# Performance work log

Hardware: AMD Instinct MI355X
Metric: run time of the kernel (lower is better)

Reference implementation:

```python
import jax, jax.numpy as jnp
import numpy as np

B, T, C = 4, 2048, 1024
N_HEAD = 16
HEAD_DIM = C // N_HEAD
SCALE = 1.0 / np.sqrt(HEAD_DIM).astype(np.float32)


def setup_inputs() -> dict:
    key = jax.random.key(0)
    k1, k2, k3 = jax.random.split(key, 3)
    x = jax.random.normal(k1, (B, T, C), dtype=jnp.float32)
    # torch Linear weights: [out_features, in_features], scaled init
    w_qkv = jax.random.normal(k2, (3 * C, C), dtype=jnp.float32) * (1.0 / np.sqrt(C))
    w_out = jax.random.normal(k3, (C, C), dtype=jnp.float32) * (1.0 / np.sqrt(C))
    b_out = jnp.zeros((C,), dtype=jnp.float32)
    return {"x": x, "w_qkv": w_qkv, "w_out": w_out, "b_out": b_out}


def reference(x, w_qkv, w_out, b_out):
    Bsz, Tlen, Cdim = x.shape
    qkv = jnp.einsum('btc,oc->bto', x, w_qkv)  # [B,T,3C]
    q, k, v = jnp.split(qkv, 3, axis=-1)
    # [B,H,T,D]
    def heads(t):
        return t.reshape(Bsz, Tlen, N_HEAD, HEAD_DIM).transpose(0, 2, 1, 3)
    q, k, v = heads(q), heads(k), heads(v)
    att = jnp.einsum('bhqd,bhkd->bhqk', q, k) * SCALE  # [B,H,T,T]
    causal = jnp.tril(jnp.ones((Tlen, Tlen), dtype=bool))
    att = jnp.where(causal[None, None], att, -jnp.inf)
    att = jax.nn.softmax(att, axis=-1)
    out = jnp.einsum('bhqk,bhkd->bhqd', att, v)
    out = out.transpose(0, 2, 1, 3).reshape(Bsz, Tlen, Cdim)
    out = jnp.einsum('btc,oc->bto', out, w_out) + b_out
    return out
```

## Files before the change

### kernel.cpp

```cpp
#include <hip/hip_runtime.h>
#include <stdint.h>


typedef __attribute__((ext_vector_type(8))) short bf16x8;
typedef __attribute__((ext_vector_type(4))) float f32x4;

#define EXP2F(x) __builtin_amdgcn_exp2f(x)
#define SL2E 0.18033688011112042f
#define FIXED_M 15.0f

template <bool B> struct BoolC { static constexpr bool value = B; };
template <int I> struct IntC { static constexpr int value = I; };

__device__ __forceinline__ short f2bf(float f) {
  union { float f; unsigned u; } c; c.f = f;
  unsigned u = c.u;
  unsigned r = (u + 0x7fffu + ((u >> 16) & 1u)) >> 16;
  return (short)(unsigned short)r;
}

__device__ __forceinline__ void softmax_pack(const f32x4* sc, bf16x8& pa0, bf16x8& pa1) {
  union U { int i[4]; bf16x8 v; };
  U u0, u1;
#pragma unroll
  for (int j = 0; j < 4; ++j) {
    float p0 = EXP2F(sc[j][0]);
    float p1 = EXP2F(sc[j][1]);
    float p2 = EXP2F(sc[j][2]);
    float p3 = EXP2F(sc[j][3]);
    int w0, w1;
    asm("v_cvt_pk_bf16_f32 %0, %1, %2" : "=v"(w0) : "v"(p0), "v"(p1));
    asm("v_cvt_pk_bf16_f32 %0, %1, %2" : "=v"(w1) : "v"(p2), "v"(p3));
    if (j < 2) { u0.i[j * 2] = w0; u0.i[j * 2 + 1] = w1; }
    else       { u1.i[(j - 2) * 2] = w0; u1.i[(j - 2) * 2 + 1] = w1; }
  }
  pa0 = u0.v;
  pa1 = u1.v;
}

__device__ __forceinline__ void llds16(const short* g, short* l) {
  __builtin_amdgcn_global_load_lds(
      (const __attribute__((address_space(1))) unsigned int*)g,
      (__attribute__((address_space(3))) unsigned int*)l, 16, 0, 0);
}

__global__ __launch_bounds__(256) void cast_all(
    const float* __restrict__ x, const float* __restrict__ wq,
    const float* __restrict__ wo, short* __restrict__ xb,
    short* __restrict__ wqb, short* __restrict__ wob) {
  const int b = blockIdx.x;
  const float* src;
  short* dst;
  int idx;
  if (b < 8192)        { src = x;  dst = xb;  idx = b * 256 + threadIdx.x; }
  else if (b < 11264)  { src = wq; dst = wqb; idx = (b - 8192) * 256 + threadIdx.x; }
  else                 { src = wo; dst = wob; idx = (b - 11264) * 256 + threadIdx.x; }
  float4 f = ((const float4*)src)[idx];
  short4 o;
  o.x = f2bf(f.x); o.y = f2bf(f.y); o.z = f2bf(f.z); o.w = f2bf(f.w);
  ((short4*)dst)[idx] = o;
}

__global__ __launch_bounds__(512) void gemm_qkv(
    const short* __restrict__ A, const short* __restrict__ Bw,
    short* __restrict__ Qo, short* __restrict__ Ko, short* __restrict__ Vt) {
  const int K = 1024;
  __shared__ short smem[73728];
  const int tid = threadIdx.x;
  const int lane = tid & 63;
  const int wave = tid >> 6;
  const int wr = wave >> 1;
  const int wc = wave & 1;
  const int m0 = blockIdx.y * 256;
  const int n0 = blockIdx.x * 128;
  const int mrow = lane & 15;
  const int kq = lane >> 4;

  f32x4 acc[4][4];
#pragma unroll
  for (int i = 0; i < 4; ++i)
#pragma unroll
    for (int j = 0; j < 4; ++j) acc[i][j] = (f32x4){0.f, 0.f, 0.f, 0.f};

  auto stageA = [&](int t, int buf, int ca) {
    const int c = ca * 512 + tid;
    const int row = c >> 3;
    const int sc = (c & 7) ^ (row & 7);
    llds16(A + (size_t)(m0 + row) * K + t * 64 + sc * 8,
           &smem[buf * 24576 + c * 8]);
  };
  auto stageB = [&](int t, int buf, int cb) {
    const int c = cb * 512 + tid;
    const int row = c >> 3;
    const int sc = (c & 7) ^ (row & 7);
    llds16(Bw + (size_t)(n0 + row) * K + t * 64 + sc * 8,
           &smem[buf * 24576 + 16384 + c * 8]);
  };

  auto rdA = [&](const short* lA, int i, int kk) -> bf16x8 {
    const int row = wr * 64 + i * 16 + mrow;
    const int ch = (kq + 4 * kk) ^ (row & 7);
    return *(const bf16x8*)&lA[row * 64 + ch * 8];
  };
  auto rdB = [&](const short* lB, int j, int kk) -> bf16x8 {
    const int row = wc * 64 + j * 16 + mrow;
    const int ch = (kq + 4 * kk) ^ (row & 7);
    return *(const bf16x8*)&lB[row * 64 + ch * 8];
  };

  stageA(0, 0, 0); stageA(0, 0, 1); stageA(0, 0, 2); stageA(0, 0, 3);
  stageB(0, 0, 0); stageB(0, 0, 1);
  stageA(1, 1, 0); stageA(1, 1, 1); stageA(1, 1, 2); stageA(1, 1, 3);
  stageB(1, 1, 0); stageB(1, 1, 1);
  asm volatile("s_waitcnt vmcnt(6)" ::: "memory");
  __builtin_amdgcn_s_barrier();

#define PHASE_TAIL()                                         \
  __builtin_amdgcn_s_barrier();                              \
  asm volatile("s_waitcnt lgkmcnt(0)" ::: "memory");         \
  __builtin_amdgcn_sched_barrier(0);                         \
  __builtin_amdgcn_s_setprio(1);

#define PHASE_END()                                          \
  __builtin_amdgcn_s_setprio(0);                             \
  __builtin_amdgcn_sched_barrier(0);                         \
  __builtin_amdgcn_s_barrier();

  for (int t = 0; t < 16; ++t) {
    const int bufi = t % 3;
    const int nb = (t + 2) % 3;
    const short* lA = &smem[bufi * 24576];
    const short* lB = lA + 16384;
    bf16x8 a0, a1, a2, a3, bf0, bf1, bf2, bf3;

    a0 = rdA(lA, 0, 0); a1 = rdA(lA, 1, 0);
    bf0 = rdB(lB, 0, 0); bf1 = rdB(lB, 1, 0);
    bf2 = rdB(lB, 2, 0); bf3 = rdB(lB, 3, 0);
    if (t < 14) { stageA(t + 2, nb, 0); stageA(t + 2, nb, 1); }
    PHASE_TAIL();
    acc[0][0] = __builtin_amdgcn_mfma_f32_16x16x32_bf16(a0, bf0, acc[0][0], 0, 0, 0);
    acc[0][1] = __builtin_amdgcn_mfma_f32_16x16x32_bf16(a0, bf1, acc[0][1], 0, 0, 0);
    acc[0][2] = __builtin_amdgcn_mfma_f32_16x16x32_bf16(a0, bf2, acc[0][2], 0, 0, 0);
    acc[0][3] = __builtin_amdgcn_mfma_f32_16x16x32_bf16(a0, bf3, acc[0][3], 0, 0, 0);
    acc[1][0] = __builtin_amdgcn_mfma_f32_16x16x32_bf16(a1, bf0, acc[1][0], 0, 0, 0);
    acc[1][1] = __builtin_amdgcn_mfma_f32_16x16x32_bf16(a1, bf1, acc[1][1], 0, 0, 0);
    acc[1][2] = __builtin_amdgcn_mfma_f32_16x16x32_bf16(a1, bf2, acc[1][2], 0, 0, 0);
    acc[1][3] = __builtin_amdgcn_mfma_f32_16x16x32_bf16(a1, bf3, acc[1][3], 0, 0, 0);
    PHASE_END();

    a2 = rdA(lA, 2, 0); a3 = rdA(lA, 3, 0);
    if (t < 14) { stageA(t + 2, nb, 2); stageA(t + 2, nb, 3); }
    PHASE_TAIL();
    acc[2][0] = __builtin_amdgcn_mfma_f32_16x16x32_bf16(a2, bf0, acc[2][0], 0, 0, 0);
    acc[2][1] = __builtin_amdgcn_mfma_f32_16x16x32_bf16(a2, bf1, acc[2][1], 0, 0, 0);
    acc[2][2] = __builtin_amdgcn_mfma_f32_16x16x32_bf16(a2, bf2, acc[2][2], 0, 0, 0);
    acc[2][3] = __builtin_amdgcn_mfma_f32_16x16x32_bf16(a2, bf3, acc[2][3], 0, 0, 0);
    acc[3][0] = __builtin_amdgcn_mfma_f32_16x16x32_bf16(a3, bf0, acc[3][0], 0, 0, 0);
    acc[3][1] = __builtin_amdgcn_mfma_f32_16x16x32_bf16(a3, bf1, acc[3][1], 0, 0, 0);
    acc[3][2] = __builtin_amdgcn_mfma_f32_16x16x32_bf16(a3, bf2, acc[3][2], 0, 0, 0);
    acc[3][3] = __builtin_amdgcn_mfma_f32_16x16x32_bf16(a3, bf3, acc[3][3], 0, 0, 0);
    PHASE_END();

    a0 = rdA(lA, 0, 1); a1 = rdA(lA, 1, 1);
    bf0 = rdB(lB, 0, 1); bf1 = rdB(lB, 1, 1);
    bf2 = rdB(lB, 2, 1); bf3 = rdB(lB, 3, 1);
    if (t < 14) { stageB(t + 2, nb, 0); stageB(t + 2, nb, 1); }
    PHASE_TAIL();
    acc[0][0] = __builtin_amdgcn_mfma_f32_16x16x32_bf16(a0, bf0, acc[0][0], 0, 0, 0);
    acc[0][1] = __builtin_amdgcn_mfma_f32_16x16x32_bf16(a0, bf1, acc[0][1], 0, 0, 0);
    acc[0][2] = __builtin_amdgcn_mfma_f32_16x16x32_bf16(a0, bf2, acc[0][2], 0, 0, 0);
    acc[0][3] = __builtin_amdgcn_mfma_f32_16x16x32_bf16(a0, bf3, acc[0][3], 0, 0, 0);
    acc[1][0] = __builtin_amdgcn_mfma_f32_16x16x32_bf16(a1, bf0, acc[1][0], 0, 0, 0);
    acc[1][1] = __builtin_amdgcn_mfma_f32_16x16x32_bf16(a1, bf1, acc[1][1], 0, 0, 0);
    acc[1][2] = __builtin_amdgcn_mfma_f32_16x16x32_bf16(a1, bf2, acc[1][2], 0, 0, 0);
    acc[1][3] = __builtin_amdgcn_mfma_f32_16x16x32_bf16(a1, bf3, acc[1][3], 0, 0, 0);
    PHASE_END();

    a2 = rdA(lA, 2, 1); a3 = rdA(lA, 3, 1);
    PHASE_TAIL();
    acc[2][0] = __builtin_amdgcn_mfma_f32_16x16x32_bf16(a2, bf0, acc[2][0], 0, 0, 0);
    acc[2][1] = __builtin_amdgcn_mfma_f32_16x16x32_bf16(a2, bf1, acc[2][1], 0, 0, 0);
    acc[2][2] = __builtin_amdgcn_mfma_f32_16x16x32_bf16(a2, bf2, acc[2][2], 0, 0, 0);
    acc[2][3] = __builtin_amdgcn_mfma_f32_16x16x32_bf16(a2, bf3, acc[2][3], 0, 0, 0);
    acc[3][0] = __builtin_amdgcn_mfma_f32_16x16x32_bf16(a3, bf0, acc[3][0], 0, 0, 0);
    acc[3][1] = __builtin_amdgcn_mfma_f32_16x16x32_bf16(a3, bf1, acc[3][1], 0, 0, 0);
    acc[3][2] = __builtin_amdgcn_mfma_f32_16x16x32_bf16(a3, bf2, acc[3][2], 0, 0, 0);
    acc[3][3] = __builtin_amdgcn_mfma_f32_16x16x32_bf16(a3, bf3, acc[3][3], 0, 0, 0);
    __builtin_amdgcn_s_setprio(0);
    __builtin_amdgcn_sched_barrier(0);
    if (t <= 13)      asm volatile("s_waitcnt vmcnt(6)" ::: "memory");
    else if (t == 14) asm volatile("s_waitcnt vmcnt(0)" ::: "memory");
    __builtin_amdgcn_s_barrier();
  }
#undef PHASE_TAIL
#undef PHASE_END

  __syncthreads();

  const int b = m0 >> 11;
  if (n0 < 2048) {
    const float sc_ = ((n0 >> 10) == 1) ? SL2E : 1.0f;
    short* lC = smem;
#pragma unroll
    for (int i = 0; i < 4; ++i) {
      const int rl = wr * 64 + i * 16 + kq * 4;
#pragma unroll
      for (int j = 0; j < 4; ++j) {
        const int col = wc * 64 + j * 16 + mrow;
#pragma unroll
        for (int r = 0; r < 4; ++r)
          lC[(rl + r) * 132 + col] = f2bf(acc[i][j][r] * sc_);
      }
    }
    __syncthreads();
    short* dst = (n0 >> 10) == 0 ? Qo : Ko;
#pragma unroll
    for (int call = 0; call < 8; ++call) {
      const int cc = call * 512 + tid;
      const int row = cc >> 4;
      const int ch = cc & 15;
      const int t = (m0 & 2047) + row;
      const int c = (n0 + ch * 8) & 1023;
      const int h = c >> 6;
      const int d = c & 63;
      bf16x8 val = *(const bf16x8*)&lC[row * 132 + ch * 8];
      *(bf16x8*)(dst + ((size_t)(b * 16 + h) * 2048 + t) * 64 + d) = val;
    }
  } else {
    short* lCt = smem;
#pragma unroll
    for (int i = 0; i < 4; ++i) {
      const int rl = wr * 64 + i * 16 + kq * 4;
#pragma unroll
      for (int j = 0; j < 4; ++j) {
        const int col = wc * 64 + j * 16 + mrow;
#pragma unroll
        for (int r = 0; r < 4; ++r)
          lCt[col * 264 + rl + r] = f2bf(acc[i][j][r]);
      }
    }
    __syncthreads();
#pragma unroll
    for (int call = 0; call < 8; ++call) {
      const int cc = call * 512 + tid;
      const int col = cc >> 5;
      const int tg = cc & 31;
      const int o = n0 + col;
      const int d = o & 63;
      const int h = (o >> 6) & 15;
      const int t = (m0 & 2047) + tg * 8;
      bf16x8 val = *(const bf16x8*)&lCt[col * 264 + tg * 8];
      *(bf16x8*)(Vt + ((size_t)(b * 16 + h) * 64 + d) * 2048 + t) = val;
    }
  }
}

__global__ __launch_bounds__(512) void gemm_out(
    const short* __restrict__ A, const short* __restrict__ Bw,
    const float* __restrict__ bias, float* __restrict__ Out) {
  const int K = 1024;
  __shared__ short smem[73728];
  const int tid = threadIdx.x;
  const int lane = tid & 63;
  const int wave = tid >> 6;
  const int wr = wave >> 1;
  const int wc = wave & 1;
  const int m0 = blockIdx.y * 256;
  const int n0 = blockIdx.x * 128;
  const int mrow = lane & 15;
  const int kq = lane >> 4;

  f32x4 acc[4][4];
#pragma unroll
  for (int i = 0; i < 4; ++i)
#pragma unroll
    for (int j = 0; j < 4; ++j) acc[i][j] = (f32x4){0.f, 0.f, 0.f, 0.f};

  auto stageA = [&](int t, int buf, int ca) {
    const int c = ca * 512 + tid;
    const int row = c >> 3;
    const int sc = (c & 7) ^ (row & 7);
    llds16(A + (size_t)(m0 + row) * K + t * 64 + sc * 8,
           &smem[buf * 24576 + c * 8]);
  };
  auto stageB = [&](int t, int buf, int cb) {
    const int c = cb * 512 + tid;
    const int row = c >> 3;
    const int sc = (c & 7) ^ (row & 7);
    llds16(Bw + (size_t)(n0 + row) * K + t * 64 + sc * 8,
           &smem[buf * 24576 + 16384 + c * 8]);
  };

  auto rdA = [&](const short* lA, int i, int kk) -> bf16x8 {
    const int row = wr * 64 + i * 16 + mrow;
    const int ch = (kq + 4 * kk) ^ (row & 7);
    return *(const bf16x8*)&lA[row * 64 + ch * 8];
  };
  auto rdB = [&](const short* lB, int j, int kk) -> bf16x8 {
    const int row = wc * 64 + j * 16 + mrow;
    const int ch = (kq + 4 * kk) ^ (row & 7);
    return *(const bf16x8*)&lB[row * 64 + ch * 8];
  };

  stageA(0, 0, 0); stageA(0, 0, 1); stageA(0, 0, 2); stageA(0, 0, 3);
  stageB(0, 0, 0); stageB(0, 0, 1);
  stageA(1, 1, 0); stageA(1, 1, 1); stageA(1, 1, 2); stageA(1, 1, 3);
  stageB(1, 1, 0); stageB(1, 1, 1);
  asm volatile("s_waitcnt vmcnt(6)" ::: "memory");
  __builtin_amdgcn_s_barrier();

#define PHASE_TAIL()                                         \
  __builtin_amdgcn_s_barrier();                              \
  asm volatile("s_waitcnt lgkmcnt(0)" ::: "memory");         \
  __builtin_amdgcn_sched_barrier(0);                         \
  __builtin_amdgcn_s_setprio(1);

#define PHASE_END()                                          \
  __builtin_amdgcn_s_setprio(0);                             \
  __builtin_amdgcn_sched_barrier(0);                         \
  __builtin_amdgcn_s_barrier();

  for (int t = 0; t < 16; ++t) {
    const int bufi = t % 3;
    const int nb = (t + 2) % 3;
    const short* lA = &smem[bufi * 24576];
    const short* lB = lA + 16384;
    bf16x8 a0, a1, a2, a3, bf0, bf1, bf2, bf3;

    a0 = rdA(lA, 0, 0); a1 = rdA(lA, 1, 0);
    bf0 = rdB(lB, 0, 0); bf1 = rdB(lB, 1, 0);
    bf2 = rdB(lB, 2, 0); bf3 = rdB(lB, 3, 0);
    if (t < 14) { stageA(t + 2, nb, 0); stageA(t + 2, nb, 1); }
    PHASE_TAIL();
    acc[0][0] = __builtin_amdgcn_mfma_f32_16x16x32_bf16(a0, bf0, acc[0][0], 0, 0, 0);
    acc[0][1] = __builtin_amdgcn_mfma_f32_16x16x32_bf16(a0, bf1, acc[0][1], 0, 0, 0);
    acc[0][2] = __builtin_amdgcn_mfma_f32_16x16x32_bf16(a0, bf2, acc[0][2], 0, 0, 0);
    acc[0][3] = __builtin_amdgcn_mfma_f32_16x16x32_bf16(a0, bf3, acc[0][3], 0, 0, 0);
    acc[1][0] = __builtin_amdgcn_mfma_f32_16x16x32_bf16(a1, bf0, acc[1][0], 0, 0, 0);
    acc[1][1] = __builtin_amdgcn_mfma_f32_16x16x32_bf16(a1, bf1, acc[1][1], 0, 0, 0);
    acc[1][2] = __builtin_amdgcn_mfma_f32_16x16x32_bf16(a1, bf2, acc[1][2], 0, 0, 0);
    acc[1][3] = __builtin_amdgcn_mfma_f32_16x16x32_bf16(a1, bf3, acc[1][3], 0, 0, 0);
    PHASE_END();

    a2 = rdA(lA, 2, 0); a3 = rdA(lA, 3, 0);
    if (t < 14) { stageA(t + 2, nb, 2); stageA(t + 2, nb, 3); }
    PHASE_TAIL();
    acc[2][0] = __builtin_amdgcn_mfma_f32_16x16x32_bf16(a2, bf0, acc[2][0], 0, 0, 0);
    acc[2][1] = __builtin_amdgcn_mfma_f32_16x16x32_bf16(a2, bf1, acc[2][1], 0, 0, 0);
    acc[2][2] = __builtin_amdgcn_mfma_f32_16x16x32_bf16(a2, bf2, acc[2][2], 0, 0, 0);
    acc[2][3] = __builtin_amdgcn_mfma_f32_16x16x32_bf16(a2, bf3, acc[2][3], 0, 0, 0);
    acc[3][0] = __builtin_amdgcn_mfma_f32_16x16x32_bf16(a3, bf0, acc[3][0], 0, 0, 0);
    acc[3][1] = __builtin_amdgcn_mfma_f32_16x16x32_bf16(a3, bf1, acc[3][1], 0, 0, 0);
    acc[3][2] = __builtin_amdgcn_mfma_f32_16x16x32_bf16(a3, bf2, acc[3][2], 0, 0, 0);
    acc[3][3] = __builtin_amdgcn_mfma_f32_16x16x32_bf16(a3, bf3, acc[3][3], 0, 0, 0);
    PHASE_END();

    a0 = rdA(lA, 0, 1); a1 = rdA(lA, 1, 1);
    bf0 = rdB(lB, 0, 1); bf1 = rdB(lB, 1, 1);
    bf2 = rdB(lB, 2, 1); bf3 = rdB(lB, 3, 1);
    if (t < 14) { stageB(t + 2, nb, 0); stageB(t + 2, nb, 1); }
    PHASE_TAIL();
    acc[0][0] = __builtin_amdgcn_mfma_f32_16x16x32_bf16(a0, bf0, acc[0][0], 0, 0, 0);
    acc[0][1] = __builtin_amdgcn_mfma_f32_16x16x32_bf16(a0, bf1, acc[0][1], 0, 0, 0);
    acc[0][2] = __builtin_amdgcn_mfma_f32_16x16x32_bf16(a0, bf2, acc[0][2], 0, 0, 0);
    acc[0][3] = __builtin_amdgcn_mfma_f32_16x16x32_bf16(a0, bf3, acc[0][3], 0, 0, 0);
    acc[1][0] = __builtin_amdgcn_mfma_f32_16x16x32_bf16(a1, bf0, acc[1][0], 0, 0, 0);
    acc[1][1] = __builtin_amdgcn_mfma_f32_16x16x32_bf16(a1, bf1, acc[1][1], 0, 0, 0);
    acc[1][2] = __builtin_amdgcn_mfma_f32_16x16x32_bf16(a1, bf2, acc[1][2], 0, 0, 0);
    acc[1][3] = __builtin_amdgcn_mfma_f32_16x16x32_bf16(a1, bf3, acc[1][3], 0, 0, 0);
    PHASE_END();

    a2 = rdA(lA, 2, 1); a3 = rdA(lA, 3, 1);
    PHASE_TAIL();
    acc[2][0] = __builtin_amdgcn_mfma_f32_16x16x32_bf16(a2, bf0, acc[2][0], 0, 0, 0);
    acc[2][1] = __builtin_amdgcn_mfma_f32_16x16x32_bf16(a2, bf1, acc[2][1], 0, 0, 0);
    acc[2][2] = __builtin_amdgcn_mfma_f32_16x16x32_bf16(a2, bf2, acc[2][2], 0, 0, 0);
    acc[2][3] = __builtin_amdgcn_mfma_f32_16x16x32_bf16(a2, bf3, acc[2][3], 0, 0, 0);
    acc[3][0] = __builtin_amdgcn_mfma_f32_16x16x32_bf16(a3, bf0, acc[3][0], 0, 0, 0);
    acc[3][1] = __builtin_amdgcn_mfma_f32_16x16x32_bf16(a3, bf1, acc[3][1], 0, 0, 0);
    acc[3][2] = __builtin_amdgcn_mfma_f32_16x16x32_bf16(a3, bf2, acc[3][2], 0, 0, 0);
    acc[3][3] = __builtin_amdgcn_mfma_f32_16x16x32_bf16(a3, bf3, acc[3][3], 0, 0, 0);
    __builtin_amdgcn_s_setprio(0);
    __builtin_amdgcn_sched_barrier(0);
    if (t <= 13)      asm volatile("s_waitcnt vmcnt(6)" ::: "memory");
    else if (t == 14) asm volatile("s_waitcnt vmcnt(0)" ::: "memory");
    __builtin_amdgcn_s_barrier();
  }
#undef PHASE_TAIL
#undef PHASE_END

#pragma unroll
  for (int i = 0; i < 4; ++i) {
    const int m = m0 + wr * 64 + i * 16 + kq * 4;
#pragma unroll
    for (int j = 0; j < 4; ++j) {
      const int n = n0 + wc * 64 + j * 16 + mrow;
      const float bb = bias[n];
#pragma unroll
      for (int r = 0; r < 4; ++r)
        Out[(size_t)(m + r) * 1024 + n] = acc[i][j][r] + bb;
    }
  }
}

__global__ __launch_bounds__(256) void flash_attn(
    const short* __restrict__ Qg, const short* __restrict__ Kg,
    const short* __restrict__ Vtg, short* __restrict__ Og) {
  const int T = 2048;
  __shared__ short lK[2][64 * 64];
  __shared__ short lVt[2][64 * 64];
  const int tid = threadIdx.x;
  const int lane = tid & 63;
  const int wave = tid >> 6;
  const int bh = blockIdx.x;
  const int bx = blockIdx.y;
  const int mrow = lane & 15;
  const int kq = lane >> 4;
  const int swz = mrow & 7;
  const size_t base = (size_t)bh * T * 64;
  const size_t vbase = (size_t)bh * 64 * T;

  int qts[4];
  qts[0] = bx;
  qts[1] = 31 - bx;
  qts[2] = 15 - bx;
  qts[3] = 16 + bx;

  const bf16x8 ones = {0x3F80, 0x3F80, 0x3F80, 0x3F80, 0x3F80, 0x3F80, 0x3F80, 0x3F80};

  bf16x8 aq0[4], aq1[4];
#pragma unroll
  for (int s = 0; s < 4; ++s) {
    const short* qp = Qg + base + (size_t)(qts[s] * 64 + wave * 16 + mrow) * 64 + kq * 8;
    aq0[s] = *(const bf16x8*)qp;
    aq1[s] = *(const bf16x8*)(qp + 32);
  }

  f32x4 acc[4][4], lac[4];
#pragma unroll
  for (int s = 0; s < 4; ++s) {
    lac[s] = (f32x4){0.f, 0.f, 0.f, 0.f};
#pragma unroll
    for (int jd = 0; jd < 4; ++jd) acc[s][jd] = (f32x4){0.f, 0.f, 0.f, 0.f};
  }

  auto stage = [&](int nt, int buf) {
#pragma unroll
    for (int call = 0; call < 2; ++call) {
      const int cb = call * 256 + wave * 64;
      const int c = cb + lane;
      const int row = c >> 3;
      const int scol = (c & 7) ^ (row & 7);
      const int grow = (row & 0x23) | ((row & 0x0C) << 1) | ((row & 0x10) >> 2);
      llds16(Kg + base + (size_t)(nt * 64 + grow) * 64 + scol * 8, &lK[buf][cb * 8]);
      llds16(Vtg + vbase + (size_t)row * T + nt * 64 + scol * 8, &lVt[buf][cb * 8]);
    }
  };

  auto seg = [&](auto Aa, auto Pi, const short* K_, const short* Vt_, int kt) {
    constexpr bool ACT0 = decltype(Aa)::value;
    constexpr int pi = decltype(Pi)::value;
    f32x4 sc0[4], sc1[4];
#pragma unroll
    for (int j = 0; j < 4; ++j) {
      const short* krow = &K_[(j * 16 + mrow) * 64];
      bf16x8 kb0 = *(const bf16x8*)&krow[(kq ^ swz) * 8];
      bf16x8 kb1 = *(const bf16x8*)&krow[((4 + kq) ^ swz) * 8];
      __builtin_amdgcn_s_setprio(1);
      f32x4 ss = (f32x4){-FIXED_M, -FIXED_M, -FIXED_M, -FIXED_M};
      ss = __builtin_amdgcn_mfma_f32_16x16x32_bf16(kb0, aq0[pi + 1], ss, 0, 0, 0);
      ss = __builtin_amdgcn_mfma_f32_16x16x32_bf16(kb1, aq1[pi + 1], ss, 0, 0, 0);
      sc1[j] = ss;
      if constexpr (ACT0) {
        f32x4 s2 = (f32x4){-FIXED_M, -FIXED_M, -FIXED_M, -FIXED_M};
        s2 = __builtin_amdgcn_mfma_f32_16x16x32_bf16(kb0, aq0[pi], s2, 0, 0, 0);
        s2 = __builtin_amdgcn_mfma_f32_16x16x32_bf16(kb1, aq1[pi], s2, 0, 0, 0);
        sc0[j] = s2;
      }
      __builtin_amdgcn_s_setprio(0);
    }

    if (kt == qts[pi + 1]) {
      const int qcol = qts[pi + 1] * 64 + wave * 16 + mrow;
#pragma unroll
      for (int j = 0; j < 4; ++j) {
        const int keyb = kt * 64 + ((j & 2) << 4) + (kq << 3) + ((j & 1) << 2);
#pragma unroll
        for (int r = 0; r < 4; ++r)
          if (keyb + r > qcol) sc1[j][r] = -1e30f;
      }
    }
    if constexpr (ACT0) {
      if (kt == qts[pi]) {
        const int qcol = qts[pi] * 64 + wave * 16 + mrow;
#pragma unroll
        for (int j = 0; j < 4; ++j) {
          const int keyb = kt * 64 + ((j & 2) << 4) + (kq << 3) + ((j & 1) << 2);
#pragma unroll
          for (int r = 0; r < 4; ++r)
            if (keyb + r > qcol) sc0[j][r] = -1e30f;
        }
      }
    }

    bf16x8 pa0_1, pa1_1, pa0_0, pa1_0;
    softmax_pack(sc1, pa0_1, pa1_1);
    lac[pi + 1] = __builtin_amdgcn_mfma_f32_16x16x32_bf16(pa0_1, ones, lac[pi + 1], 0, 0, 0);
    lac[pi + 1] = __builtin_amdgcn_mfma_f32_16x16x32_bf16(pa1_1, ones, lac[pi + 1], 0, 0, 0);
    if constexpr (ACT0) {
      softmax_pack(sc0, pa0_0, pa1_0);
      lac[pi] = __builtin_amdgcn_mfma_f32_16x16x32_bf16(pa0_0, ones, lac[pi], 0, 0, 0);
      lac[pi] = __builtin_amdgcn_mfma_f32_16x16x32_bf16(pa1_0, ones, lac[pi], 0, 0, 0);
    }

#pragma unroll
    for (int jd = 0; jd < 4; ++jd) {
      const short* vrow = &Vt_[(jd * 16 + mrow) * 64];
      bf16x8 vb0 = *(const bf16x8*)&vrow[(kq ^ swz) * 8];
      bf16x8 vb1 = *(const bf16x8*)&vrow[((4 + kq) ^ swz) * 8];
      __builtin_amdgcn_s_setprio(1);
      acc[pi + 1][jd] = __builtin_amdgcn_mfma_f32_16x16x32_bf16(pa0_1, vb0, acc[pi + 1][jd], 0, 0, 0);
      acc[pi + 1][jd] = __builtin_amdgcn_mfma_f32_16x16x32_bf16(pa1_1, vb1, acc[pi + 1][jd], 0, 0, 0);
      if constexpr (ACT0) {
        acc[pi][jd] = __builtin_amdgcn_mfma_f32_16x16x32_bf16(pa0_0, vb0, acc[pi][jd], 0, 0, 0);
        acc[pi][jd] = __builtin_amdgcn_mfma_f32_16x16x32_bf16(pa1_0, vb1, acc[pi][jd], 0, 0, 0);
      }
      __builtin_amdgcn_s_setprio(0);
    }
  };

  stage(0, 0);
  const int ktmax = qts[1];
  for (int kt = 0; kt <= ktmax; ++kt) {
    const int bcur = kt & 1;
    if (kt < ktmax) {
      stage(kt + 1, bcur ^ 1);
      asm volatile("s_waitcnt vmcnt(4)" ::: "memory");
    } else {
      asm volatile("s_waitcnt vmcnt(0)" ::: "memory");
    }
    __builtin_amdgcn_s_barrier();
    const short* K_ = lK[bcur];
    const short* Vt_ = lVt[bcur];
    if (kt <= qts[0]) seg(BoolC<true>{}, IntC<0>{}, K_, Vt_, kt);
    else              seg(BoolC<false>{}, IntC<0>{}, K_, Vt_, kt);
    if (kt <= qts[3]) {
      if (kt <= qts[2]) seg(BoolC<true>{}, IntC<1 * 2>{}, K_, Vt_, kt);
      else              seg(BoolC<false>{}, IntC<1 * 2>{}, K_, Vt_, kt);
    }
    __builtin_amdgcn_s_barrier();
  }

  const int b = bh >> 4;
  const int h = bh & 15;
#pragma unroll
  for (int s = 0; s < 4; ++s) {
#pragma unroll
    for (int r = 0; r < 4; ++r) {
      const float inv = 1.0f / lac[s][r];
      const int t = qts[s] * 64 + wave * 16 + kq * 4 + r;
#pragma unroll
      for (int jd = 0; jd < 4; ++jd) {
        const int col = h * 64 + jd * 16 + mrow;
        Og[((size_t)b * 2048 + t) * 1024 + col] = f2bf(acc[s][jd][r] * inv);
      }
    }
  }
}

extern "C" void kernel_launch(void* const* d_in, const int* in_sizes, int n_in,
                              void* d_out, int out_size, void* d_ws, size_t ws_size,
                              hipStream_t stream) {
  const float* x = (const float*)d_in[0];
  const float* w_qkv = (const float*)d_in[1];
  const float* w_out = (const float*)d_in[2];
  const float* b_out = (const float*)d_in[3];
  float* out = (float*)d_out;

  char* ws = (char*)d_ws;
  const size_t NX = 8192ull * 1024;
  const size_t NWQ = 3072ull * 1024;
  const size_t NWO = 1024ull * 1024;
  const size_t NQ = 64ull * 2048 * 64;
  size_t off = 0;
  short* xb    = (short*)(ws + off); off += NX * 2;
  short* wqkvb = (short*)(ws + off); off += NWQ * 2;
  short* woutb = (short*)(ws + off); off += NWO * 2;
  short* q     = (short*)(ws + off); off += NQ * 2;
  short* k     = (short*)(ws + off); off += NQ * 2;
  short* vt    = (short*)(ws + off); off += NQ * 2;
  short* attb  = (short*)(ws + off); off += NX * 2;
  if (off > ws_size) return;

  cast_all<<<12288, 256, 0, stream>>>(x, w_qkv, w_out, xb, wqkvb, woutb);
  gemm_qkv<<<dim3(24, 32), 512, 0, stream>>>(xb, wqkvb, q, k, vt);
  flash_attn<<<dim3(64, 8), 256, 0, stream>>>(q, k, vt, attb);
  gemm_out<<<dim3(8, 32), 512, 0, stream>>>(attb, woutb, b_out, out);
}
```

Baseline: 243.0 us.

## Enlarge QKV GEMM tile to 256x256 with double-buffered LDS pipeline

```diff
diff --git a/kernel.cpp b/kernel.cpp
--- a/kernel.cpp
+++ b/kernel.cpp
@@ -65,20 +65,20 @@
     const short* __restrict__ A, const short* __restrict__ Bw,
     short* __restrict__ Qo, short* __restrict__ Ko, short* __restrict__ Vt) {
   const int K = 1024;
-  __shared__ short smem[73728];
+  __shared__ short smem[65536];
   const int tid = threadIdx.x;
   const int lane = tid & 63;
   const int wave = tid >> 6;
-  const int wr = wave >> 1;
-  const int wc = wave & 1;
+  const int wr = wave >> 2;
+  const int wc = wave & 3;
   const int m0 = blockIdx.y * 256;
-  const int n0 = blockIdx.x * 128;
+  const int n0 = blockIdx.x * 256;
   const int mrow = lane & 15;
   const int kq = lane >> 4;
 
-  f32x4 acc[4][4];
-#pragma unroll
-  for (int i = 0; i < 4; ++i)
+  f32x4 acc[8][4];
+#pragma unroll
+  for (int i = 0; i < 8; ++i)
 #pragma unroll
     for (int j = 0; j < 4; ++j) acc[i][j] = (f32x4){0.f, 0.f, 0.f, 0.f};
 
@@ -87,18 +87,18 @@
     const int row = c >> 3;
     const int sc = (c & 7) ^ (row & 7);
     llds16(A + (size_t)(m0 + row) * K + t * 64 + sc * 8,
-           &smem[buf * 24576 + c * 8]);
+           &smem[buf * 32768 + c * 8]);
   };
   auto stageB = [&](int t, int buf, int cb) {
     const int c = cb * 512 + tid;
     const int row = c >> 3;
     const int sc = (c & 7) ^ (row & 7);
     llds16(Bw + (size_t)(n0 + row) * K + t * 64 + sc * 8,
-           &smem[buf * 24576 + 16384 + c * 8]);
+           &smem[buf * 32768 + 16384 + c * 8]);
   };
 
   auto rdA = [&](const short* lA, int i, int kk) -> bf16x8 {
-    const int row = wr * 64 + i * 16 + mrow;
+    const int row = wr * 128 + i * 16 + mrow;
     const int ch = (kq + 4 * kk) ^ (row & 7);
     return *(const bf16x8*)&lA[row * 64 + ch * 8];
   };
@@ -109,11 +109,9 @@
   };
 
   stageA(0, 0, 0); stageA(0, 0, 1); stageA(0, 0, 2); stageA(0, 0, 3);
-  stageB(0, 0, 0); stageB(0, 0, 1);
-  stageA(1, 1, 0); stageA(1, 1, 1); stageA(1, 1, 2); stageA(1, 1, 3);
-  stageB(1, 1, 0); stageB(1, 1, 1);
-  asm volatile("s_waitcnt vmcnt(6)" ::: "memory");
-  __builtin_amdgcn_s_barrier();
+  stageB(0, 0, 0); stageB(0, 0, 1); stageB(0, 0, 2); stageB(0, 0, 3);
+  asm volatile("s_waitcnt vmcnt(0)" ::: "memory");
+  __syncthreads();
 
 #define PHASE_TAIL()                                         \
   __builtin_amdgcn_s_barrier();                              \
@@ -126,72 +124,60 @@
   __builtin_amdgcn_sched_barrier(0);                         \
   __builtin_amdgcn_s_barrier();
 
+#define MFMA16(I0)                                                             \
+  acc[I0+0][0] = __builtin_amdgcn_mfma_f32_16x16x32_bf16(a0, bf0, acc[I0+0][0], 0, 0, 0); \
+  acc[I0+0][1] = __builtin_amdgcn_mfma_f32_16x16x32_bf16(a0, bf1, acc[I0+0][1], 0, 0, 0); \
+  acc[I0+0][2] = __builtin_amdgcn_mfma_f32_16x16x32_bf16(a0, bf2, acc[I0+0][2], 0, 0, 0); \
+  acc[I0+0][3] = __builtin_amdgcn_mfma_f32_16x16x32_bf16(a0, bf3, acc[I0+0][3], 0, 0, 0); \
+  acc[I0+1][0] = __builtin_amdgcn_mfma_f32_16x16x32_bf16(a1, bf0, acc[I0+1][0], 0, 0, 0); \
+  acc[I0+1][1] = __builtin_amdgcn_mfma_f32_16x16x32_bf16(a1, bf1, acc[I0+1][1], 0, 0, 0); \
+  acc[I0+1][2] = __builtin_amdgcn_mfma_f32_16x16x32_bf16(a1, bf2, acc[I0+1][2], 0, 0, 0); \
+  acc[I0+1][3] = __builtin_amdgcn_mfma_f32_16x16x32_bf16(a1, bf3, acc[I0+1][3], 0, 0, 0); \
+  acc[I0+2][0] = __builtin_amdgcn_mfma_f32_16x16x32_bf16(a2, bf0, acc[I0+2][0], 0, 0, 0); \
+  acc[I0+2][1] = __builtin_amdgcn_mfma_f32_16x16x32_bf16(a2, bf1, acc[I0+2][1], 0, 0, 0); \
+  acc[I0+2][2] = __builtin_amdgcn_mfma_f32_16x16x32_bf16(a2, bf2, acc[I0+2][2], 0, 0, 0); \
+  acc[I0+2][3] = __builtin_amdgcn_mfma_f32_16x16x32_bf16(a2, bf3, acc[I0+2][3], 0, 0, 0); \
+  acc[I0+3][0] = __builtin_amdgcn_mfma_f32_16x16x32_bf16(a3, bf0, acc[I0+3][0], 0, 0, 0); \
+  acc[I0+3][1] = __builtin_amdgcn_mfma_f32_16x16x32_bf16(a3, bf1, acc[I0+3][1], 0, 0, 0); \
+  acc[I0+3][2] = __builtin_amdgcn_mfma_f32_16x16x32_bf16(a3, bf2, acc[I0+3][2], 0, 0, 0); \
+  acc[I0+3][3] = __builtin_amdgcn_mfma_f32_16x16x32_bf16(a3, bf3, acc[I0+3][3], 0, 0, 0);
+
   for (int t = 0; t < 16; ++t) {
-    const int bufi = t % 3;
-    const int nb = (t + 2) % 3;
-    const short* lA = &smem[bufi * 24576];
+    const int buf = t & 1;
+    const int nb = buf ^ 1;
+    const short* lA = &smem[buf * 32768];
     const short* lB = lA + 16384;
     bf16x8 a0, a1, a2, a3, bf0, bf1, bf2, bf3;
 
-    a0 = rdA(lA, 0, 0); a1 = rdA(lA, 1, 0);
-    bf0 = rdB(lB, 0, 0); bf1 = rdB(lB, 1, 0);
-    bf2 = rdB(lB, 2, 0); bf3 = rdB(lB, 3, 0);
-    if (t < 14) { stageA(t + 2, nb, 0); stageA(t + 2, nb, 1); }
-    PHASE_TAIL();
-    acc[0][0] = __builtin_amdgcn_mfma_f32_16x16x32_bf16(a0, bf0, acc[0][0], 0, 0, 0);
-    acc[0][1] = __builtin_amdgcn_mfma_f32_16x16x32_bf16(a0, bf1, acc[0][1], 0, 0, 0);
-    acc[0][2] = __builtin_amdgcn_mfma_f32_16x16x32_bf16(a0, bf2, acc[0][2], 0, 0, 0);
-    acc[0][3] = __builtin_amdgcn_mfma_f32_16x16x32_bf16(a0, bf3, acc[0][3], 0, 0, 0);
-    acc[1][0] = __builtin_amdgcn_mfma_f32_16x16x32_bf16(a1, bf0, acc[1][0], 0, 0, 0);
-    acc[1][1] = __builtin_amdgcn_mfma_f32_16x16x32_bf16(a1, bf1, acc[1][1], 0, 0, 0);
-    acc[1][2] = __builtin_amdgcn_mfma_f32_16x16x32_bf16(a1, bf2, acc[1][2], 0, 0, 0);
-    acc[1][3] = __builtin_amdgcn_mfma_f32_16x16x32_bf16(a1, bf3, acc[1][3], 0, 0, 0);
+    a0 = rdA(lA, 0, 0); a1 = rdA(lA, 1, 0); a2 = rdA(lA, 2, 0); a3 = rdA(lA, 3, 0);
+    bf0 = rdB(lB, 0, 0); bf1 = rdB(lB, 1, 0); bf2 = rdB(lB, 2, 0); bf3 = rdB(lB, 3, 0);
+    if (t < 15) { stageA(t + 1, nb, 0); stageA(t + 1, nb, 1); stageA(t + 1, nb, 2); }
+    PHASE_TAIL();
+    MFMA16(0);
     PHASE_END();
 
-    a2 = rdA(lA, 2, 0); a3 = rdA(lA, 3, 0);
-    if (t < 14) { stageA(t + 2, nb, 2); stageA(t + 2, nb, 3); }
-    PHASE_TAIL();
-    acc[2][0] = __builtin_amdgcn_mfma_f32_16x16x32_bf16(a2, bf0, acc[2][0], 0, 0, 0);
-    acc[2][1] = __builtin_amdgcn_mfma_f32_16x16x32_bf16(a2, bf1, acc[2][1], 0, 0, 0);
-    acc[2][2] = __builtin_amdgcn_mfma_f32_16x16x32_bf16(a2, bf2, acc[2][2], 0, 0, 0);
-    acc[2][3] = __builtin_amdgcn_mfma_f32_16x16x32_bf16(a2, bf3, acc[2][3], 0, 0, 0);
-    acc[3][0] = __builtin_amdgcn_mfma_f32_16x16x32_bf16(a3, bf0, acc[3][0], 0, 0, 0);
-    acc[3][1] = __builtin_amdgcn_mfma_f32_16x16x32_bf16(a3, bf1, acc[3][1], 0, 0, 0);
-    acc[3][2] = __builtin_amdgcn_mfma_f32_16x16x32_bf16(a3, bf2, acc[3][2], 0, 0, 0);
-    acc[3][3] = __builtin_amdgcn_mfma_f32_16x16x32_bf16(a3, bf3, acc[3][3], 0, 0, 0);
+    a0 = rdA(lA, 4, 0); a1 = rdA(lA, 5, 0); a2 = rdA(lA, 6, 0); a3 = rdA(lA, 7, 0);
+    if (t < 15) { stageA(t + 1, nb, 3); stageB(t + 1, nb, 0); stageB(t + 1, nb, 1); }
+    PHASE_TAIL();
+    MFMA16(4);
     PHASE_END();
 
-    a0 = rdA(lA, 0, 1); a1 = rdA(lA, 1, 1);
-    bf0 = rdB(lB, 0, 1); bf1 = rdB(lB, 1, 1);
-    bf2 = rdB(lB, 2, 1); bf3 = rdB(lB, 3, 1);
-    if (t < 14) { stageB(t + 2, nb, 0); stageB(t + 2, nb, 1); }
-    PHASE_TAIL();
-    acc[0][0] = __builtin_amdgcn_mfma_f32_16x16x32_bf16(a0, bf0, acc[0][0], 0, 0, 0);
-    acc[0][1] = __builtin_amdgcn_mfma_f32_16x16x32_bf16(a0, bf1, acc[0][1], 0, 0, 0);
-    acc[0][2] = __builtin_amdgcn_mfma_f32_16x16x32_bf16(a0, bf2, acc[0][2], 0, 0, 0);
-    acc[0][3] = __builtin_amdgcn_mfma_f32_16x16x32_bf16(a0, bf3, acc[0][3], 0, 0, 0);
-    acc[1][0] = __builtin_amdgcn_mfma_f32_16x16x32_bf16(a1, bf0, acc[1][0], 0, 0, 0);
-    acc[1][1] = __builtin_amdgcn_mfma_f32_16x16x32_bf16(a1, bf1, acc[1][1], 0, 0, 0);
-    acc[1][2] = __builtin_amdgcn_mfma_f32_16x16x32_bf16(a1, bf2, acc[1][2], 0, 0, 0);
-    acc[1][3] = __builtin_amdgcn_mfma_f32_16x16x32_bf16(a1, bf3, acc[1][3], 0, 0, 0);
+    a0 = rdA(lA, 0, 1); a1 = rdA(lA, 1, 1); a2 = rdA(lA, 2, 1); a3 = rdA(lA, 3, 1);
+    bf0 = rdB(lB, 0, 1); bf1 = rdB(lB, 1, 1); bf2 = rdB(lB, 2, 1); bf3 = rdB(lB, 3, 1);
+    if (t < 15) { stageB(t + 1, nb, 2); stageB(t + 1, nb, 3); }
+    PHASE_TAIL();
+    MFMA16(0);
     PHASE_END();
 
-    a2 = rdA(lA, 2, 1); a3 = rdA(lA, 3, 1);
-    PHASE_TAIL();
-    acc[2][0] = __builtin_amdgcn_mfma_f32_16x16x32_bf16(a2, bf0, acc[2][0], 0, 0, 0);
-    acc[2][1] = __builtin_amdgcn_mfma_f32_16x16x32_bf16(a2, bf1, acc[2][1], 0, 0, 0);
-    acc[2][2] = __builtin_amdgcn_mfma_f32_16x16x32_bf16(a2, bf2, acc[2][2], 0, 0, 0);
-    acc[2][3] = __builtin_amdgcn_mfma_f32_16x16x32_bf16(a2, bf3, acc[2][3], 0, 0, 0);
-    acc[3][0] = __builtin_amdgcn_mfma_f32_16x16x32_bf16(a3, bf0, acc[3][0], 0, 0, 0);
-    acc[3][1] = __builtin_amdgcn_mfma_f32_16x16x32_bf16(a3, bf1, acc[3][1], 0, 0, 0);
-    acc[3][2] = __builtin_amdgcn_mfma_f32_16x16x32_bf16(a3, bf2, acc[3][2], 0, 0, 0);
-    acc[3][3] = __builtin_amdgcn_mfma_f32_16x16x32_bf16(a3, bf3, acc[3][3], 0, 0, 0);
+    a0 = rdA(lA, 4, 1); a1 = rdA(lA, 5, 1); a2 = rdA(lA, 6, 1); a3 = rdA(lA, 7, 1);
+    PHASE_TAIL();
+    MFMA16(4);
     __builtin_amdgcn_s_setprio(0);
     __builtin_amdgcn_sched_barrier(0);
-    if (t <= 13)      asm volatile("s_waitcnt vmcnt(6)" ::: "memory");
-    else if (t == 14) asm volatile("s_waitcnt vmcnt(0)" ::: "memory");
+    if (t < 15) asm volatile("s_waitcnt vmcnt(0)" ::: "memory");
     __builtin_amdgcn_s_barrier();
   }
+#undef MFMA16
 #undef PHASE_TAIL
 #undef PHASE_END
 
@@ -201,56 +187,68 @@
   if (n0 < 2048) {
     const float sc_ = ((n0 >> 10) == 1) ? SL2E : 1.0f;
     short* lC = smem;
-#pragma unroll
-    for (int i = 0; i < 4; ++i) {
-      const int rl = wr * 64 + i * 16 + kq * 4;
-#pragma unroll
-      for (int j = 0; j < 4; ++j) {
-        const int col = wc * 64 + j * 16 + mrow;
-#pragma unroll
-        for (int r = 0; r < 4; ++r)
-          lC[(rl + r) * 132 + col] = f2bf(acc[i][j][r] * sc_);
-      }
-    }
-    __syncthreads();
     short* dst = (n0 >> 10) == 0 ? Qo : Ko;
-#pragma unroll
-    for (int call = 0; call < 8; ++call) {
-      const int cc = call * 512 + tid;
-      const int row = cc >> 4;
-      const int ch = cc & 15;
-      const int t = (m0 & 2047) + row;
-      const int c = (n0 + ch * 8) & 1023;
-      const int h = c >> 6;
-      const int d = c & 63;
-      bf16x8 val = *(const bf16x8*)&lC[row * 132 + ch * 8];
-      *(bf16x8*)(dst + ((size_t)(b * 16 + h) * 2048 + t) * 64 + d) = val;
+#pragma unroll 1
+    for (int p = 0; p < 2; ++p) {
+      if (p) __syncthreads();
+      if (wr == p) {
+#pragma unroll
+        for (int i = 0; i < 8; ++i) {
+          const int rl = i * 16 + kq * 4;
+#pragma unroll
+          for (int j = 0; j < 4; ++j) {
+            const int col = wc * 64 + j * 16 + mrow;
+#pragma unroll
+            for (int r = 0; r < 4; ++r)
+              lC[(rl + r) * 260 + col] = f2bf(acc[i][j][r] * sc_);
+          }
+        }
+      }
+      __syncthreads();
+#pragma unroll
+      for (int call = 0; call < 8; ++call) {
+        const int cc = call * 512 + tid;
+        const int row = cc >> 5;
+        const int ch = cc & 31;
+        const int t = (m0 & 2047) + p * 128 + row;
+        const int c = (n0 + ch * 8) & 1023;
+        const int h = c >> 6;
+        const int d = c & 63;
+        bf16x8 val = *(const bf16x8*)&lC[row * 260 + ch * 8];
+        *(bf16x8*)(dst + ((size_t)(b * 16 + h) * 2048 + t) * 64 + d) = val;
+      }
     }
   } else {
     short* lCt = smem;
-#pragma unroll
-    for (int i = 0; i < 4; ++i) {
-      const int rl = wr * 64 + i * 16 + kq * 4;
-#pragma unroll
-      for (int j = 0; j < 4; ++j) {
-        const int col = wc * 64 + j * 16 + mrow;
-#pragma unroll
-        for (int r = 0; r < 4; ++r)
-          lCt[col * 264 + rl + r] = f2bf(acc[i][j][r]);
-      }
-    }
-    __syncthreads();
-#pragma unroll
-    for (int call = 0; call < 8; ++call) {
-      const int cc = call * 512 + tid;
-      const int col = cc >> 5;
-      const int tg = cc & 31;
-      const int o = n0 + col;
-      const int d = o & 63;
-      const int h = (o >> 6) & 15;
-      const int t = (m0 & 2047) + tg * 8;
-      bf16x8 val = *(const bf16x8*)&lCt[col * 264 + tg * 8];
-      *(bf16x8*)(Vt + ((size_t)(b * 16 + h) * 64 + d) * 2048 + t) = val;
+#pragma unroll 1
+    for (int p = 0; p < 2; ++p) {
+      if (p) __syncthreads();
+      if (wr == p) {
+#pragma unroll
+        for (int i = 0; i < 8; ++i) {
+          const int rl = i * 16 + kq * 4;
+#pragma unroll
+          for (int j = 0; j < 4; ++j) {
+            const int col = wc * 64 + j * 16 + mrow;
+#pragma unroll
+            for (int r = 0; r < 4; ++r)
+              lCt[col * 136 + rl + r] = f2bf(acc[i][j][r]);
+          }
+        }
+      }
+      __syncthreads();
+#pragma unroll
+      for (int call = 0; call < 8; ++call) {
+        const int cc = call * 512 + tid;
+        const int col = cc >> 4;
+        const int tg = cc & 15;
+        const int o = n0 + col;
+        const int d = o & 63;
+        const int h = (o >> 6) & 15;
+        const int t = (m0 & 2047) + p * 128 + tg * 8;
+        bf16x8 val = *(const bf16x8*)&lCt[col * 136 + tg * 8];
+        *(bf16x8*)(Vt + ((size_t)(b * 16 + h) * 64 + d) * 2048 + t) = val;
+      }
     }
   }
 }
@@ -593,7 +591,7 @@
   if (off > ws_size) return;
 
   cast_all<<<12288, 256, 0, stream>>>(x, w_qkv, w_out, xb, wqkvb, woutb);
-  gemm_qkv<<<dim3(24, 32), 512, 0, stream>>>(xb, wqkvb, q, k, vt);
+  gemm_qkv<<<dim3(12, 32), 512, 0, stream>>>(xb, wqkvb, q, k, vt);
   flash_attn<<<dim3(64, 8), 256, 0, stream>>>(q, k, vt, attb);
   gemm_out<<<dim3(8, 32), 512, 0, stream>>>(attb, woutb, b_out, out);
 }
```

Result: no change. 242.6 us (-0.2%).
